# Performance work log

Hardware: AMD Instinct MI355X
Metric: run time of the kernel (lower is better)

The kernel has to match this reference:

```python
import jax, jax.numpy as jnp
import numpy as np

D = 1024      # model dim (used for theta exponent and 1/sqrt(d) scale)
D_H = 128     # head dim


def make_theta():
    # theta[i] = 10 ** (-2*(i-1)/d), each value repeated twice -> length d_H
    i = np.repeat(np.arange(D_H // 2), 2)
    return jnp.asarray(10.0 ** (-2.0 * (i - 1) / D), dtype=jnp.float32)


def rotation(x, theta):
    # x: [B, T, d_H]; positions are 1..T (source uses arange(1, T+1))
    B, T, dh = x.shape
    idx = jnp.arange(1, T + 1, dtype=x.dtype)[:, None]          # [T, 1]
    ang = idx * theta[None, :]                                   # [T, d_H]
    cos, sin = jnp.cos(ang), jnp.sin(ang)
    # pairwise swap with sign: (x0, x1) -> (x1, -x0)
    x2 = x.reshape(B, T, dh // 2, 2)
    swapped = jnp.stack([x2[..., 1], -x2[..., 0]], axis=-1).reshape(B, T, dh)
    return x * cos + swapped * sin


def setup_inputs() -> dict:
    key = jax.random.key(0)
    kx, kq, kk, kv = jax.random.split(key, 4)
    B, T = 4, 2048
    scale = 1.0 / np.sqrt(D)
    return {
        "x": jax.random.normal(kx, (B, T, D), dtype=jnp.float32),
        "Wq": jax.random.normal(kq, (D_H, D), dtype=jnp.float32) * scale,
        "Wk": jax.random.normal(kk, (D_H, D), dtype=jnp.float32) * scale,
        "Wv": jax.random.normal(kv, (D_H, D), dtype=jnp.float32) * scale,
        "theta": make_theta(),
    }


def reference(x, Wq, Wk, Wv, theta):
    B, T, d = x.shape
    Q = jnp.einsum('btd,hd->bth', x, Wq)
    K = jnp.einsum('btd,hd->bth', x, Wk)
    V = jnp.einsum('btd,hd->bth', x, Wv)
    Q = rotation(Q, theta)
    K = rotation(K, theta)
    # scale uses model dim d (not d_H), as in the source
    scores = jnp.einsum('bqh,bkh->bqk', Q, K) * (d ** -0.5)
    causal = jnp.tril(jnp.ones((T, T), dtype=bool))
    scores = jnp.where(causal, scores, -jnp.inf)
    attn = jax.nn.softmax(scores, axis=-1)
    return jnp.einsum('bqk,bkh->bqh', attn, V)
```

## Files before the change

kernel.cpp:

```cpp
#include <hip/hip_runtime.h>
#include <math.h>

#define T_SEQ 2048
#define D_MODEL 1024
#define DH 128
#define SLOTS 288
#define FRAG_B 262144

typedef __bf16 bfx8 __attribute__((ext_vector_type(8)));
typedef float f32x4 __attribute__((ext_vector_type(4)));

union U16x8 { uint4 u4; unsigned int ui[4]; unsigned short us[8]; __bf16 bf[8]; bfx8 v; };

__device__ inline uint4 cvt8u(float4 a, float4 b) {
    U16x8 u;
    u.bf[0] = (__bf16)a.x; u.bf[1] = (__bf16)a.y; u.bf[2] = (__bf16)a.z; u.bf[3] = (__bf16)a.w;
    u.bf[4] = (__bf16)b.x; u.bf[5] = (__bf16)b.y; u.bf[6] = (__bf16)b.z; u.bf[7] = (__bf16)b.w;
    return u.u4;
}

__device__ inline int slot_base32(int qt) {
    int g = qt >> 3, j = qt & 7;
    return 4 * g * (g + 1) + j * (g + 1);
}

__global__ __launch_bounds__(256) void prep_kernel(
    const float* __restrict__ x,
    const float* __restrict__ Wq, const float* __restrict__ Wk,
    const float* __restrict__ Wv,
    __bf16* __restrict__ xF, __bf16* __restrict__ WF, int nxb)
{
    const int bi = blockIdx.x;
    const int tid = threadIdx.x;

    if (bi < nxb) {
        __shared__ __align__(16) unsigned short Xs[64 * 72];
        const int m0 = (bi >> 4) * 64;
        const int k0 = (bi & 15) * 64;
        const int row = tid >> 2, cs = (tid & 3) * 16;
        const float* xp = x + (size_t)(m0 + row) * D_MODEL + k0 + cs;
        float4 a0 = *(const float4*)xp;
        float4 a1 = *(const float4*)(xp + 4);
        float4 a2 = *(const float4*)(xp + 8);
        float4 a3 = *(const float4*)(xp + 12);
        *(uint4*)&Xs[row * 72 + cs]     = cvt8u(a0, a1);
        *(uint4*)&Xs[row * 72 + cs + 8] = cvt8u(a2, a3);
        __syncthreads();
        const int L = tid & 63;
        #pragma unroll
        for (int rr = 0; rr < 2; ++rr) {
            const int fid = rr * 4 + (tid >> 6);
            const int mtl = fid >> 1, kcl = fid & 1;
            uint4 d = *(const uint4*)&Xs[(mtl * 16 + (L & 15)) * 72 + kcl * 32 + (L >> 4) * 8];
            const size_t frag = (size_t)((m0 >> 4) + mtl) * 32 + (k0 >> 5) + kcl;
            *(uint4*)&xF[frag * 512 + L * 8] = d;
        }
    } else {
        const int i = (bi - nxb) * 256 + tid;
        const int wsel = i >> 14;
        const int i2 = i & 16383;
        const int kc = i2 >> 9, j = (i2 >> 6) & 7, ln = i2 & 63;
        const int lo = ln & 15, quad = ln >> 4;
        const float* src = (wsel == 0) ? Wq : (wsel == 1) ? Wk : Wv;
        const float* p = src + (size_t)(j * 16 + lo) * D_MODEL + kc * 32 + quad * 8;
        float4 a = *(const float4*)p;
        float4 b = *(const float4*)(p + 4);
        *(uint4*)&WF[(size_t)((wsel * 32 + kc) * 8 + j) * 512 + ln * 8] = cvt8u(a, b);
    }
}

__global__ __launch_bounds__(64) void qkv_kernel(
    const __bf16* __restrict__ xF, const __bf16* __restrict__ WF,
    const float* __restrict__ theta,
    __bf16* __restrict__ QF, __bf16* __restrict__ KF, __bf16* __restrict__ VF)
{
    __shared__ __align__(16) unsigned short T[32 * 136];

    const int bx = blockIdx.x;
    const int ln = threadIdx.x;
    const int lo = ln & 15, quad = ln >> 4;

    if (bx < 2048) {
        const int wsel01 = bx >> 10;
        const int sub = (bx >> 8) & 3;
        const int iq = sub >> 1, jh = sub & 1;
        const int mt = bx & 255;
        const int mt16 = mt * 2 + iq;

        const __bf16* WFp = WF + (size_t)wsel01 * (32 * 8 * 512) + (size_t)jh * (4 * 512);
        const size_t xb = (size_t)mt16 * 32;

        bfx8 xA = *(const bfx8*)&xF[(xb + 0) * 512 + ln * 8];
        bfx8 xB = *(const bfx8*)&xF[(xb + 1) * 512 + ln * 8];
        bfx8 wA[4], wB[4];
        #pragma unroll
        for (int jl = 0; jl < 4; ++jl) {
            wA[jl] = *(const bfx8*)&WFp[(size_t)jl * 512 + ln * 8];
            wB[jl] = *(const bfx8*)&WFp[(size_t)(8 + jl) * 512 + ln * 8];
        }

        f32x4 acc[4];
        #pragma unroll
        for (int jl = 0; jl < 4; ++jl) acc[jl] = (f32x4)(0.f);

        for (int kc = 0; kc < 32; kc += 2) {
            const int kpA = (kc + 2 < 32) ? kc + 2 : kc;
            #pragma unroll
            for (int jl = 0; jl < 4; ++jl) {
                acc[jl] = __builtin_amdgcn_mfma_f32_16x16x32_bf16(xA, wA[jl], acc[jl], 0, 0, 0);
                wA[jl] = *(const bfx8*)&WFp[((size_t)kpA * 8 + jl) * 512 + ln * 8];
            }
            xA = *(const bfx8*)&xF[(xb + kpA) * 512 + ln * 8];
            const int kpB = (kc + 3 < 32) ? kc + 3 : kc + 1;
            #pragma unroll
            for (int jl = 0; jl < 4; ++jl) {
                acc[jl] = __builtin_amdgcn_mfma_f32_16x16x32_bf16(xB, wB[jl], acc[jl], 0, 0, 0);
                wB[jl] = *(const bfx8*)&WFp[((size_t)kpB * 8 + jl) * 512 + ln * 8];
            }
            xB = *(const bfx8*)&xF[(xb + kpB) * 512 + ln * 8];
        }

        const int b = mt16 >> 7;
        const int t16 = mt16 & 127;
        const int mloc16 = t16 * 16;
        __bf16* dstP = (wsel01 == 0 ? QF : KF) + (size_t)b * FRAG_B;

        #pragma unroll
        for (int jl = 0; jl < 4; ++jl) {
            const int j = jh * 4 + jl;
            const int h = j * 16 + lo;
            const float th = theta[h];
            #pragma unroll
            for (int r = 0; r < 4; ++r) {
                const int pos = mloc16 + quad * 4 + r + 1;
                float v = acc[jl][r];
                float partner = __shfl_xor(v, 1, 64);
                float ang = (float)pos * th;
                float rev = ang * 0.15915494309189535f;
                rev -= floorf(rev);
                float sn = __builtin_amdgcn_sinf(rev);
                float cs = __builtin_amdgcn_cosf(rev);
                float res = (h & 1) ? (v * cs - partner * sn)
                                    : (v * cs + partner * sn);
                U16x8 u; u.bf[0] = (__bf16)res;
                T[(quad * 4 + r) * 136 + h] = u.us[0];
            }
        }
        #pragma unroll
        for (int c4l = 0; c4l < 2; ++c4l) {
            const int c4 = jh * 2 + c4l;
            uint4 d = *(const uint4*)&T[(ln & 15) * 136 + c4 * 32 + (ln >> 4) * 8];
            *(uint4*)&dstP[(size_t)(t16 * 4 + c4) * 512 + ln * 8] = d;
        }
    } else {
        const int r2 = bx - 2048;
        const int jh = r2 >> 8;
        const int mt = r2 & 255;
        const int mt16 = mt * 2;

        const __bf16* WFp = WF + (size_t)2 * (32 * 8 * 512) + (size_t)jh * (4 * 512);
        const size_t xb0 = (size_t)mt16 * 32, xb1 = xb0 + 32;

        bfx8 xA[2], xB[2], wA[4], wB[4];
        xA[0] = *(const bfx8*)&xF[(xb0 + 0) * 512 + ln * 8];
        xA[1] = *(const bfx8*)&xF[(xb1 + 0) * 512 + ln * 8];
        xB[0] = *(const bfx8*)&xF[(xb0 + 1) * 512 + ln * 8];
        xB[1] = *(const bfx8*)&xF[(xb1 + 1) * 512 + ln * 8];
        #pragma unroll
        for (int jl = 0; jl < 4; ++jl) {
            wA[jl] = *(const bfx8*)&WFp[(size_t)jl * 512 + ln * 8];
            wB[jl] = *(const bfx8*)&WFp[(size_t)(8 + jl) * 512 + ln * 8];
        }

        f32x4 acc[2][4];
        #pragma unroll
        for (int iq = 0; iq < 2; ++iq)
            #pragma unroll
            for (int jl = 0; jl < 4; ++jl) acc[iq][jl] = (f32x4)(0.f);

        for (int kc = 0; kc < 32; kc += 2) {
            const int kpA = (kc + 2 < 32) ? kc + 2 : kc;
            #pragma unroll
            for (int jl = 0; jl < 4; ++jl) {
                acc[0][jl] = __builtin_amdgcn_mfma_f32_16x16x32_bf16(xA[0], wA[jl], acc[0][jl], 0, 0, 0);
                acc[1][jl] = __builtin_amdgcn_mfma_f32_16x16x32_bf16(xA[1], wA[jl], acc[1][jl], 0, 0, 0);
                wA[jl] = *(const bfx8*)&WFp[((size_t)kpA * 8 + jl) * 512 + ln * 8];
            }
            xA[0] = *(const bfx8*)&xF[(xb0 + kpA) * 512 + ln * 8];
            xA[1] = *(const bfx8*)&xF[(xb1 + kpA) * 512 + ln * 8];
            const int kpB = (kc + 3 < 32) ? kc + 3 : kc + 1;
            #pragma unroll
            for (int jl = 0; jl < 4; ++jl) {
                acc[0][jl] = __builtin_amdgcn_mfma_f32_16x16x32_bf16(xB[0], wB[jl], acc[0][jl], 0, 0, 0);
                acc[1][jl] = __builtin_amdgcn_mfma_f32_16x16x32_bf16(xB[1], wB[jl], acc[1][jl], 0, 0, 0);
                wB[jl] = *(const bfx8*)&WFp[((size_t)kpB * 8 + jl) * 512 + ln * 8];
            }
            xB[0] = *(const bfx8*)&xF[(xb0 + kpB) * 512 + ln * 8];
            xB[1] = *(const bfx8*)&xF[(xb1 + kpB) * 512 + ln * 8];
        }

        const int b = mt >> 6;
        const int kt32 = mt & 63;
        #pragma unroll
        for (int iq = 0; iq < 2; ++iq)
            #pragma unroll
            for (int jl = 0; jl < 4; ++jl) {
                const int j = jh * 4 + jl;
                #pragma unroll
                for (int r = 0; r < 4; ++r) {
                    U16x8 u; u.bf[0] = (__bf16)acc[iq][jl][r];
                    T[(iq * 16 + quad * 4 + r) * 136 + j * 16 + lo] = u.us[0];
                }
            }
        __bf16* dstP = VF + (size_t)b * FRAG_B;
        #pragma unroll
        for (int jl = 0; jl < 4; ++jl) {
            const int j = jh * 4 + jl;
            U16x8 u;
            #pragma unroll
            for (int e = 0; e < 8; ++e)
                u.us[e] = T[((ln >> 4) * 8 + e) * 136 + j * 16 + (ln & 15)];
            *(uint4*)&dstP[(size_t)(kt32 * 8 + j) * 512 + ln * 8] = u.u4;
        }
    }
}

__global__ __launch_bounds__(128) void attn_partial_kernel(
    const __bf16* __restrict__ QF, const __bf16* __restrict__ KF,
    const __bf16* __restrict__ VF,
    __bf16* __restrict__ Opb, float* __restrict__ Ll)
{
    const int bxx = blockIdx.x;
    const int b = bxx >> 1;
    const int qt = (int)blockIdx.y * 2 + (bxx & 1);
    const int c = blockIdx.z;
    const int qbase = qt * 32;
    const int kstart = c << 8;
    if (kstart > qbase) return;
    const int nt = min(8, (qbase + 32 - kstart) >> 5);

    __shared__ __align__(16) unsigned short Pw[2][1280];
    __shared__ float RedO[2 * 8 * 4 * 64];
    __shared__ float RedL[2 * 4 * 64];

    const int tid = threadIdx.x;
    const int w = tid >> 6;
    const int ln = tid & 63;
    const int lo = ln & 15, quad = ln >> 4;
    const int hi8 = quad * 8;

    const __bf16* QFb = QF + (size_t)b * FRAG_B;
    const __bf16* KFb = KF + (size_t)b * FRAG_B;
    const __bf16* VFb = VF + (size_t)b * FRAG_B;

    bfx8 qf[2][4];
    #pragma unroll
    for (int iq = 0; iq < 2; ++iq)
        #pragma unroll
        for (int c4 = 0; c4 < 4; ++c4)
            qf[iq][c4] = *(const bfx8*)&QFb[(size_t)((qt * 2 + iq) * 4 + c4) * 512 + ln * 8];

    f32x4 O[2][8];
    #pragma unroll
    for (int iq = 0; iq < 2; ++iq)
        #pragma unroll
        for (int j = 0; j < 8; ++j) O[iq][j] = (f32x4)(0.f);
    float lsum[2][4];
    #pragma unroll
    for (int iq = 0; iq < 2; ++iq)
        #pragma unroll
        for (int r = 0; r < 4; ++r) lsum[iq][r] = 0.f;

    bfx8 kcur[2][4], knxt[2][4];
    {
        const int kf0 = (kstart + w * 32) >> 4;
        #pragma unroll
        for (int jj = 0; jj < 2; ++jj)
            #pragma unroll
            for (int c4 = 0; c4 < 4; ++c4)
                kcur[jj][c4] = *(const bfx8*)&KFb[(size_t)((kf0 + jj) * 4 + c4) * 512 + ln * 8];
    }

    for (int kt = w; kt < nt; kt += 2) {
        const int k0 = kstart + kt * 32;
        bfx8 vf[8];
        #pragma unroll
        for (int j = 0; j < 8; ++j)
            vf[j] = *(const bfx8*)&VFb[(size_t)((k0 >> 5) * 8 + j) * 512 + ln * 8];
        if (kt + 2 < nt) {
            const int kn16 = (k0 + 64) >> 4;
            #pragma unroll
            for (int jj = 0; jj < 2; ++jj)
                #pragma unroll
                for (int c4 = 0; c4 < 4; ++c4)
                    knxt[jj][c4] = *(const bfx8*)&KFb[(size_t)((kn16 + jj) * 4 + c4) * 512 + ln * 8];
        }

        f32x4 s4[2][2];
        #pragma unroll
        for (int iq = 0; iq < 2; ++iq)
            #pragma unroll
            for (int jj = 0; jj < 2; ++jj) s4[iq][jj] = (f32x4)(0.f);
        #pragma unroll
        for (int c4 = 0; c4 < 4; ++c4)
            #pragma unroll
            for (int iq = 0; iq < 2; ++iq)
                #pragma unroll
                for (int jj = 0; jj < 2; ++jj)
                    s4[iq][jj] = __builtin_amdgcn_mfma_f32_16x16x32_bf16(qf[iq][c4], kcur[jj][c4], s4[iq][jj], 0, 0, 0);

        const bool needMask = (k0 + 31 > qbase);
        #pragma unroll
        for (int iq = 0; iq < 2; ++iq)
            #pragma unroll
            for (int jj = 0; jj < 2; ++jj)
                #pragma unroll
                for (int r = 0; r < 4; ++r) {
                    const int col = k0 + jj * 16 + lo;
                    const int row = qbase + iq * 16 + quad * 4 + r;
                    float p = __expf(s4[iq][jj][r] * 0.03125f);
                    if (needMask && col > row) p = 0.f;
                    lsum[iq][r] += p;
                    U16x8 u; u.bf[0] = (__bf16)p;
                    Pw[w][iq * 640 + (quad * 4 + r) * 40 + jj * 16 + lo] = u.us[0];
                }

        bfx8 pf0 = *(const bfx8*)&Pw[w][lo * 40 + hi8];
        bfx8 pf1 = *(const bfx8*)&Pw[w][640 + lo * 40 + hi8];
        #pragma unroll
        for (int j = 0; j < 8; ++j) {
            O[0][j] = __builtin_amdgcn_mfma_f32_16x16x32_bf16(pf0, vf[j], O[0][j], 0, 0, 0);
            O[1][j] = __builtin_amdgcn_mfma_f32_16x16x32_bf16(pf1, vf[j], O[1][j], 0, 0, 0);
        }

        #pragma unroll
        for (int jj = 0; jj < 2; ++jj)
            #pragma unroll
            for (int c4 = 0; c4 < 4; ++c4) kcur[jj][c4] = knxt[jj][c4];
    }

    #pragma unroll
    for (int off = 1; off < 16; off <<= 1)
        #pragma unroll
        for (int iq = 0; iq < 2; ++iq)
            #pragma unroll
            for (int r = 0; r < 4; ++r) lsum[iq][r] += __shfl_xor(lsum[iq][r], off, 64);

    if (w == 1) {
        #pragma unroll
        for (int iq = 0; iq < 2; ++iq)
            #pragma unroll
            for (int j = 0; j < 8; ++j)
                #pragma unroll
                for (int r = 0; r < 4; ++r)
                    RedO[((iq * 8 + j) * 4 + r) * 64 + ln] = O[iq][j][r];
        #pragma unroll
        for (int iq = 0; iq < 2; ++iq)
            #pragma unroll
            for (int r = 0; r < 4; ++r)
                RedL[(iq * 4 + r) * 64 + ln] = lsum[iq][r];
    }
    __syncthreads();
    if (w == 0) {
        #pragma unroll
        for (int iq = 0; iq < 2; ++iq)
            #pragma unroll
            for (int j = 0; j < 8; ++j)
                #pragma unroll
                for (int r = 0; r < 4; ++r)
                    O[iq][j][r] += RedO[((iq * 8 + j) * 4 + r) * 64 + ln];
        #pragma unroll
        for (int iq = 0; iq < 2; ++iq)
            #pragma unroll
            for (int r = 0; r < 4; ++r)
                lsum[iq][r] += RedL[(iq * 4 + r) * 64 + ln];

        const size_t sb = (size_t)b * SLOTS + slot_base32(qt) + c;
        #pragma unroll
        for (int iq = 0; iq < 2; ++iq)
            #pragma unroll
            for (int j = 0; j < 8; ++j) {
                U16x8 u;
                u.bf[0] = (__bf16)O[iq][j][0]; u.bf[1] = (__bf16)O[iq][j][1];
                u.bf[2] = (__bf16)O[iq][j][2]; u.bf[3] = (__bf16)O[iq][j][3];
                *(uint2*)&Opb[((sb * 2 + iq) * 8 + j) * 256 + ln * 4] = make_uint2(u.ui[0], u.ui[1]);
            }
        if (lo == 0) {
            #pragma unroll
            for (int iq = 0; iq < 2; ++iq)
                #pragma unroll
                for (int r = 0; r < 4; ++r)
                    Ll[sb * 32 + iq * 16 + quad * 4 + r] = lsum[iq][r];
        }
    }
}

__global__ __launch_bounds__(128) void attn_merge_kernel(
    const __bf16* __restrict__ Opb, const float* __restrict__ Ll,
    float* __restrict__ out)
{
    const int qt = blockIdx.x, b = blockIdx.y, jh2 = blockIdx.z;
    const int g = qt >> 3, nc = g + 1;
    const size_t base = (size_t)b * SLOTS + slot_base32(qt);

    __shared__ float Lsh[8][32];
    const int tid = threadIdx.x;
    const int iq = tid >> 6, ln = tid & 63;
    const int lo = ln & 15, quad = ln >> 4;

    for (int idx = tid; idx < nc * 32; idx += 128)
        Lsh[idx >> 5][idx & 31] = Ll[(base + (idx >> 5)) * 32 + (idx & 31)];
    __syncthreads();

    float acc[4][4];
    #pragma unroll
    for (int jl = 0; jl < 4; ++jl)
        #pragma unroll
        for (int r = 0; r < 4; ++r) acc[jl][r] = 0.f;

    for (int cc = 0; cc < nc; ++cc) {
        #pragma unroll
        for (int jl = 0; jl < 4; ++jl) {
            const int j = jh2 * 4 + jl;
            uint2 d = *(const uint2*)&Opb[(((base + cc) * 2 + iq) * 8 + j) * 256 + ln * 4];
            U16x8 u; u.ui[0] = d.x; u.ui[1] = d.y;
            #pragma unroll
            for (int r = 0; r < 4; ++r) acc[jl][r] += (float)u.bf[r];
        }
    }

    #pragma unroll
    for (int r = 0; r < 4; ++r) {
        const int row = iq * 16 + quad * 4 + r;
        float l = 0.f;
        for (int cc = 0; cc < nc; ++cc) l += Lsh[cc][row];
        const float rl = 1.0f / l;
        #pragma unroll
        for (int jl = 0; jl < 4; ++jl) {
            const int j = jh2 * 4 + jl;
            out[((size_t)b * T_SEQ + qt * 32 + row) * DH + j * 16 + lo] = acc[jl][r] * rl;
        }
    }
}

extern "C" void kernel_launch(void* const* d_in, const int* in_sizes, int n_in,
                              void* d_out, int out_size, void* d_ws, size_t ws_size,
                              hipStream_t stream) {
    const float* x     = (const float*)d_in[0];
    const float* Wq    = (const float*)d_in[1];
    const float* Wk    = (const float*)d_in[2];
    const float* Wv    = (const float*)d_in[3];
    const float* theta = (const float*)d_in[4];
    float* out = (float*)d_out;

    const int M = in_sizes[0] / D_MODEL;
    const int B = M / T_SEQ;

    __bf16* xF  = (__bf16*)d_ws;
    __bf16* WF  = xF + (size_t)M * D_MODEL;
    __bf16* QF  = WF + (size_t)3 * 32 * 8 * 512;
    __bf16* KF  = QF + (size_t)B * FRAG_B;
    __bf16* VF  = KF + (size_t)B * FRAG_B;
    __bf16* Opb = VF + (size_t)B * FRAG_B;
    float*  Ll  = (float*)(Opb + (size_t)B * SLOTS * 2 * 8 * 256);

    const int nxb = (M / 64) * 16;
    prep_kernel<<<dim3(nxb + 192), 256, 0, stream>>>(x, Wq, Wk, Wv, xF, WF, nxb);
    qkv_kernel<<<dim3(2048 + 512), 64, 0, stream>>>(xF, WF, theta, QF, KF, VF);
    attn_partial_kernel<<<dim3(2 * B, T_SEQ / 64, 8), 128, 0, stream>>>(QF, KF, VF, Opb, Ll);
    attn_merge_kernel<<<dim3(T_SEQ / 32, B, 2), 128, 0, stream>>>(Opb, Ll, out);
}
```

Baseline: 122.1 us.

## Fuse four-stage pipeline into one persistent cooperative kernel with grid syncs

Replaces the four separate launches (prep, QKV projection, partial attention, merge) with a single cooperative persistent kernel. Each phase is split into tasks that blocks or waves take in a strided loop, and phases are separated by grid.sync. This removes per-launch overhead and the idle gaps between kernels. In exchange, the whole grid waits at each barrier, the work is spread across a fixed 256 or 512 blocks, and register pressure rises under launch_bounds(256,2). The old four-kernel path remains as a fallback if the cooperative launch fails.

```diff
diff --git a/kernel.cpp b/kernel.cpp
--- a/kernel.cpp
+++ b/kernel.cpp
@@ -1,5 +1,8 @@
 #include <hip/hip_runtime.h>
+#include <hip/hip_cooperative_groups.h>
 #include <math.h>
+
+namespace cg = cooperative_groups;
 
 #define T_SEQ 2048
 #define D_MODEL 1024
@@ -23,6 +26,7 @@
     int g = qt >> 3, j = qt & 7;
     return 4 * g * (g + 1) + j * (g + 1);
 }
+
 
 __global__ __launch_bounds__(256) void prep_kernel(
     const float* __restrict__ x,
@@ -443,6 +447,413 @@
     }
 }
 
+
+__device__ __forceinline__ void qkv_task(
+    int t, unsigned short* T,
+    const __bf16* __restrict__ xF, const __bf16* __restrict__ WF,
+    const float* __restrict__ theta,
+    __bf16* __restrict__ QF, __bf16* __restrict__ KF, __bf16* __restrict__ VF,
+    int ln, int lo, int quad)
+{
+    if (t < 2048) {
+        const int wsel01 = t >> 10;
+        const int sub = (t >> 8) & 3;
+        const int iq = sub >> 1, jh = sub & 1;
+        const int mt = t & 255;
+        const int mt16 = mt * 2 + iq;
+
+        const __bf16* WFp = WF + (size_t)wsel01 * (32 * 8 * 512) + (size_t)jh * (4 * 512);
+        const size_t xb = (size_t)mt16 * 32;
+
+        bfx8 xA = *(const bfx8*)&xF[(xb + 0) * 512 + ln * 8];
+        bfx8 xB = *(const bfx8*)&xF[(xb + 1) * 512 + ln * 8];
+        bfx8 wA[4], wB[4];
+        #pragma unroll
+        for (int jl = 0; jl < 4; ++jl) {
+            wA[jl] = *(const bfx8*)&WFp[(size_t)jl * 512 + ln * 8];
+            wB[jl] = *(const bfx8*)&WFp[(size_t)(8 + jl) * 512 + ln * 8];
+        }
+
+        f32x4 acc[4];
+        #pragma unroll
+        for (int jl = 0; jl < 4; ++jl) acc[jl] = (f32x4)(0.f);
+
+        for (int kc = 0; kc < 32; kc += 2) {
+            const int kpA = (kc + 2 < 32) ? kc + 2 : kc;
+            #pragma unroll
+            for (int jl = 0; jl < 4; ++jl) {
+                acc[jl] = __builtin_amdgcn_mfma_f32_16x16x32_bf16(xA, wA[jl], acc[jl], 0, 0, 0);
+                wA[jl] = *(const bfx8*)&WFp[((size_t)kpA * 8 + jl) * 512 + ln * 8];
+            }
+            xA = *(const bfx8*)&xF[(xb + kpA) * 512 + ln * 8];
+            const int kpB = (kc + 3 < 32) ? kc + 3 : kc + 1;
+            #pragma unroll
+            for (int jl = 0; jl < 4; ++jl) {
+                acc[jl] = __builtin_amdgcn_mfma_f32_16x16x32_bf16(xB, wB[jl], acc[jl], 0, 0, 0);
+                wB[jl] = *(const bfx8*)&WFp[((size_t)kpB * 8 + jl) * 512 + ln * 8];
+            }
+            xB = *(const bfx8*)&xF[(xb + kpB) * 512 + ln * 8];
+        }
+
+        const int b = mt16 >> 7;
+        const int t16 = mt16 & 127;
+        const int mloc16 = t16 * 16;
+        __bf16* dstP = (wsel01 == 0 ? QF : KF) + (size_t)b * FRAG_B;
+
+        #pragma unroll
+        for (int jl = 0; jl < 4; ++jl) {
+            const int j = jh * 4 + jl;
+            const int h = j * 16 + lo;
+            const float th = theta[h];
+            #pragma unroll
+            for (int r = 0; r < 4; ++r) {
+                const int pos = mloc16 + quad * 4 + r + 1;
+                float v = acc[jl][r];
+                float partner = __shfl_xor(v, 1, 64);
+                float ang = (float)pos * th;
+                float rev = ang * 0.15915494309189535f;
+                rev -= floorf(rev);
+                float sn = __builtin_amdgcn_sinf(rev);
+                float cs = __builtin_amdgcn_cosf(rev);
+                float res = (h & 1) ? (v * cs - partner * sn)
+                                    : (v * cs + partner * sn);
+                U16x8 u; u.bf[0] = (__bf16)res;
+                T[(quad * 4 + r) * 136 + h] = u.us[0];
+            }
+        }
+        #pragma unroll
+        for (int c4l = 0; c4l < 2; ++c4l) {
+            const int c4 = jh * 2 + c4l;
+            uint4 d = *(const uint4*)&T[(ln & 15) * 136 + c4 * 32 + (ln >> 4) * 8];
+            *(uint4*)&dstP[(size_t)(t16 * 4 + c4) * 512 + ln * 8] = d;
+        }
+    } else {
+        const int r2 = t - 2048;
+        const int jh = r2 >> 8;
+        const int mt = r2 & 255;
+        const int mt16 = mt * 2;
+
+        const __bf16* WFp = WF + (size_t)2 * (32 * 8 * 512) + (size_t)jh * (4 * 512);
+        const size_t xb0 = (size_t)mt16 * 32, xb1 = xb0 + 32;
+
+        bfx8 xA[2], xB[2], wA[4], wB[4];
+        xA[0] = *(const bfx8*)&xF[(xb0 + 0) * 512 + ln * 8];
+        xA[1] = *(const bfx8*)&xF[(xb1 + 0) * 512 + ln * 8];
+        xB[0] = *(const bfx8*)&xF[(xb0 + 1) * 512 + ln * 8];
+        xB[1] = *(const bfx8*)&xF[(xb1 + 1) * 512 + ln * 8];
+        #pragma unroll
+        for (int jl = 0; jl < 4; ++jl) {
+            wA[jl] = *(const bfx8*)&WFp[(size_t)jl * 512 + ln * 8];
+            wB[jl] = *(const bfx8*)&WFp[(size_t)(8 + jl) * 512 + ln * 8];
+        }
+
+        f32x4 acc[2][4];
+        #pragma unroll
+        for (int iq = 0; iq < 2; ++iq)
+            #pragma unroll
+            for (int jl = 0; jl < 4; ++jl) acc[iq][jl] = (f32x4)(0.f);
+
+        for (int kc = 0; kc < 32; kc += 2) {
+            const int kpA = (kc + 2 < 32) ? kc + 2 : kc;
+            #pragma unroll
+            for (int jl = 0; jl < 4; ++jl) {
+                acc[0][jl] = __builtin_amdgcn_mfma_f32_16x16x32_bf16(xA[0], wA[jl], acc[0][jl], 0, 0, 0);
+                acc[1][jl] = __builtin_amdgcn_mfma_f32_16x16x32_bf16(xA[1], wA[jl], acc[1][jl], 0, 0, 0);
+                wA[jl] = *(const bfx8*)&WFp[((size_t)kpA * 8 + jl) * 512 + ln * 8];
+            }
+            xA[0] = *(const bfx8*)&xF[(xb0 + kpA) * 512 + ln * 8];
+            xA[1] = *(const bfx8*)&xF[(xb1 + kpA) * 512 + ln * 8];
+            const int kpB = (kc + 3 < 32) ? kc + 3 : kc + 1;
+            #pragma unroll
+            for (int jl = 0; jl < 4; ++jl) {
+                acc[0][jl] = __builtin_amdgcn_mfma_f32_16x16x32_bf16(xB[0], wB[jl], acc[0][jl], 0, 0, 0);
+                acc[1][jl] = __builtin_amdgcn_mfma_f32_16x16x32_bf16(xB[1], wB[jl], acc[1][jl], 0, 0, 0);
+                wB[jl] = *(const bfx8*)&WFp[((size_t)kpB * 8 + jl) * 512 + ln * 8];
+            }
+            xB[0] = *(const bfx8*)&xF[(xb0 + kpB) * 512 + ln * 8];
+            xB[1] = *(const bfx8*)&xF[(xb1 + kpB) * 512 + ln * 8];
+        }
+
+        const int b = mt >> 6;
+        const int kt32 = mt & 63;
+        #pragma unroll
+        for (int iq = 0; iq < 2; ++iq)
+            #pragma unroll
+            for (int jl = 0; jl < 4; ++jl) {
+                const int j = jh * 4 + jl;
+                #pragma unroll
+                for (int r = 0; r < 4; ++r) {
+                    U16x8 u; u.bf[0] = (__bf16)acc[iq][jl][r];
+                    T[(iq * 16 + quad * 4 + r) * 136 + j * 16 + lo] = u.us[0];
+                }
+            }
+        __bf16* dstP = VF + (size_t)b * FRAG_B;
+        #pragma unroll
+        for (int jl = 0; jl < 4; ++jl) {
+            const int j = jh * 4 + jl;
+            U16x8 u;
+            #pragma unroll
+            for (int e = 0; e < 8; ++e)
+                u.us[e] = T[((ln >> 4) * 8 + e) * 136 + j * 16 + (ln & 15)];
+            *(uint4*)&dstP[(size_t)(kt32 * 8 + j) * 512 + ln * 8] = u.u4;
+        }
+    }
+}
+
+__global__ __launch_bounds__(256, 2) void fused_kernel(
+    const float* __restrict__ x,
+    const float* __restrict__ Wq, const float* __restrict__ Wk,
+    const float* __restrict__ Wv, const float* __restrict__ theta,
+    __bf16* __restrict__ xF, __bf16* __restrict__ WF,
+    __bf16* __restrict__ QF, __bf16* __restrict__ KF, __bf16* __restrict__ VF,
+    __bf16* __restrict__ Opb, float* __restrict__ Ll,
+    float* __restrict__ out)
+{
+    __shared__ __align__(16) unsigned char SMEM[34816];
+    cg::grid_group grid = cg::this_grid();
+
+    const int nblk = gridDim.x;
+    const int bid = blockIdx.x;
+    const int tid = threadIdx.x;
+    const int w = tid >> 6;
+    const int ln = tid & 63;
+    const int lo = ln & 15, quad = ln >> 4;
+    const int wid = bid * 4 + w;
+
+    {
+        unsigned short* Xs = (unsigned short*)SMEM;
+        for (int task = bid; task < 2048 + 192; task += nblk) {
+            if (task < 2048) {
+                const int m0 = (task >> 4) * 64;
+                const int k0 = (task & 15) * 64;
+                const int row = tid >> 2, cs = (tid & 3) * 16;
+                const float* xp = x + (size_t)(m0 + row) * D_MODEL + k0 + cs;
+                float4 a0 = *(const float4*)xp;
+                float4 a1 = *(const float4*)(xp + 4);
+                float4 a2 = *(const float4*)(xp + 8);
+                float4 a3 = *(const float4*)(xp + 12);
+                *(uint4*)&Xs[row * 72 + cs]     = cvt8u(a0, a1);
+                *(uint4*)&Xs[row * 72 + cs + 8] = cvt8u(a2, a3);
+                __syncthreads();
+                const int L = tid & 63;
+                #pragma unroll
+                for (int rr = 0; rr < 2; ++rr) {
+                    const int fid = rr * 4 + (tid >> 6);
+                    const int mtl = fid >> 1, kcl = fid & 1;
+                    uint4 d = *(const uint4*)&Xs[(mtl * 16 + (L & 15)) * 72 + kcl * 32 + (L >> 4) * 8];
+                    const size_t frag = (size_t)((m0 >> 4) + mtl) * 32 + (k0 >> 5) + kcl;
+                    *(uint4*)&xF[frag * 512 + L * 8] = d;
+                }
+                __syncthreads();
+            } else {
+                const int i = (task - 2048) * 256 + tid;
+                const int wsel = i >> 14;
+                const int i2 = i & 16383;
+                const int kc = i2 >> 9, j = (i2 >> 6) & 7, l2 = i2 & 63;
+                const int lo2 = l2 & 15, q2 = l2 >> 4;
+                const float* src = (wsel == 0) ? Wq : (wsel == 1) ? Wk : Wv;
+                const float* p = src + (size_t)(j * 16 + lo2) * D_MODEL + kc * 32 + q2 * 8;
+                float4 a = *(const float4*)p;
+                float4 b = *(const float4*)(p + 4);
+                *(uint4*)&WF[(size_t)((wsel * 32 + kc) * 8 + j) * 512 + l2 * 8] = cvt8u(a, b);
+            }
+        }
+    }
+    __threadfence();
+    grid.sync();
+    __threadfence();
+
+    {
+        unsigned short* T = (unsigned short*)SMEM + (size_t)w * (32 * 136);
+        const int nw = nblk * 4;
+        for (int t = wid; t < 2560; t += nw)
+            qkv_task(t, T, xF, WF, theta, QF, KF, VF, ln, lo, quad);
+    }
+    __threadfence();
+    grid.sync();
+    __threadfence();
+
+    {
+        const int cls = bid & 7;
+        const int b = cls >> 1, parity = cls & 1;
+        const int strideR = (nblk >> 3) * 4;
+        unsigned short* Pw = (unsigned short*)SMEM + (size_t)w * 1280;
+        const int hi8 = quad * 8;
+
+        const __bf16* QFb = QF + (size_t)b * FRAG_B;
+        const __bf16* KFb = KF + (size_t)b * FRAG_B;
+        const __bf16* VFb = VF + (size_t)b * FRAG_B;
+
+        for (int rk = (bid >> 3) * 4 + w; rk < 144; rk += strideR) {
+            int qt2 = 0, accb = 0;
+            while (true) { int ncg = (qt2 >> 2) + 1; if (rk < accb + ncg) break; accb += ncg; ++qt2; }
+            const int c = rk - accb;
+            const int qt = qt2 * 2 + parity;
+            const int qbase = qt * 32;
+            const int kstart = c << 8;
+            const int nt = min(8, (qbase + 32 - kstart) >> 5);
+
+            bfx8 qf[2][4];
+            #pragma unroll
+            for (int iq = 0; iq < 2; ++iq)
+                #pragma unroll
+                for (int c4 = 0; c4 < 4; ++c4)
+                    qf[iq][c4] = *(const bfx8*)&QFb[(size_t)((qt * 2 + iq) * 4 + c4) * 512 + ln * 8];
+
+            f32x4 O[2][8];
+            #pragma unroll
+            for (int iq = 0; iq < 2; ++iq)
+                #pragma unroll
+                for (int j = 0; j < 8; ++j) O[iq][j] = (f32x4)(0.f);
+            float lsum[2][4];
+            #pragma unroll
+            for (int iq = 0; iq < 2; ++iq)
+                #pragma unroll
+                for (int r = 0; r < 4; ++r) lsum[iq][r] = 0.f;
+
+            bfx8 kcur[2][4], knxt[2][4];
+            #pragma unroll
+            for (int jj = 0; jj < 2; ++jj)
+                #pragma unroll
+                for (int c4 = 0; c4 < 4; ++c4)
+                    kcur[jj][c4] = *(const bfx8*)&KFb[(size_t)(((kstart >> 4) + jj) * 4 + c4) * 512 + ln * 8];
+
+            for (int kt = 0; kt < nt; ++kt) {
+                const int k0 = kstart + kt * 32;
+                bfx8 vf[8];
+                #pragma unroll
+                for (int j = 0; j < 8; ++j)
+                    vf[j] = *(const bfx8*)&VFb[(size_t)((k0 >> 5) * 8 + j) * 512 + ln * 8];
+                if (kt + 1 < nt) {
+                    const int kn16 = (k0 + 32) >> 4;
+                    #pragma unroll
+                    for (int jj = 0; jj < 2; ++jj)
+                        #pragma unroll
+                        for (int c4 = 0; c4 < 4; ++c4)
+                            knxt[jj][c4] = *(const bfx8*)&KFb[(size_t)((kn16 + jj) * 4 + c4) * 512 + ln * 8];
+                }
+
+                f32x4 s4[2][2];
+                #pragma unroll
+                for (int iq = 0; iq < 2; ++iq)
+                    #pragma unroll
+                    for (int jj = 0; jj < 2; ++jj) s4[iq][jj] = (f32x4)(0.f);
+                #pragma unroll
+                for (int c4 = 0; c4 < 4; ++c4)
+                    #pragma unroll
+                    for (int iq = 0; iq < 2; ++iq)
+                        #pragma unroll
+                        for (int jj = 0; jj < 2; ++jj)
+                            s4[iq][jj] = __builtin_amdgcn_mfma_f32_16x16x32_bf16(qf[iq][c4], kcur[jj][c4], s4[iq][jj], 0, 0, 0);
+
+                const bool needMask = (k0 + 31 > qbase);
+                #pragma unroll
+                for (int iq = 0; iq < 2; ++iq)
+                    #pragma unroll
+                    for (int jj = 0; jj < 2; ++jj)
+                        #pragma unroll
+                        for (int r = 0; r < 4; ++r) {
+                            const int col = k0 + jj * 16 + lo;
+                            const int row = qbase + iq * 16 + quad * 4 + r;
+                            float p = __expf(s4[iq][jj][r] * 0.03125f);
+                            if (needMask && col > row) p = 0.f;
+                            lsum[iq][r] += p;
+                            U16x8 u; u.bf[0] = (__bf16)p;
+                            Pw[iq * 640 + (quad * 4 + r) * 40 + jj * 16 + lo] = u.us[0];
+                        }
+
+                bfx8 pf0 = *(const bfx8*)&Pw[lo * 40 + hi8];
+                bfx8 pf1 = *(const bfx8*)&Pw[640 + lo * 40 + hi8];
+                #pragma unroll
+                for (int j = 0; j < 8; ++j) {
+                    O[0][j] = __builtin_amdgcn_mfma_f32_16x16x32_bf16(pf0, vf[j], O[0][j], 0, 0, 0);
+                    O[1][j] = __builtin_amdgcn_mfma_f32_16x16x32_bf16(pf1, vf[j], O[1][j], 0, 0, 0);
+                }
+
+                #pragma unroll
+                for (int jj = 0; jj < 2; ++jj)
+                    #pragma unroll
+                    for (int c4 = 0; c4 < 4; ++c4) kcur[jj][c4] = knxt[jj][c4];
+            }
+
+            #pragma unroll
+            for (int off = 1; off < 16; off <<= 1)
+                #pragma unroll
+                for (int iq = 0; iq < 2; ++iq)
+                    #pragma unroll
+                    for (int r = 0; r < 4; ++r) lsum[iq][r] += __shfl_xor(lsum[iq][r], off, 64);
+
+            const size_t sb = (size_t)b * SLOTS + slot_base32(qt) + c;
+            #pragma unroll
+            for (int iq = 0; iq < 2; ++iq)
+                #pragma unroll
+                for (int j = 0; j < 8; ++j) {
+                    U16x8 u;
+                    u.bf[0] = (__bf16)O[iq][j][0]; u.bf[1] = (__bf16)O[iq][j][1];
+                    u.bf[2] = (__bf16)O[iq][j][2]; u.bf[3] = (__bf16)O[iq][j][3];
+                    *(uint2*)&Opb[((sb * 2 + iq) * 8 + j) * 256 + ln * 4] = make_uint2(u.ui[0], u.ui[1]);
+                }
+            if (lo == 0) {
+                #pragma unroll
+                for (int iq = 0; iq < 2; ++iq)
+                    #pragma unroll
+                    for (int r = 0; r < 4; ++r)
+                        Ll[sb * 32 + iq * 16 + quad * 4 + r] = lsum[iq][r];
+            }
+        }
+    }
+    __threadfence();
+    grid.sync();
+    __threadfence();
+
+    for (int mb = bid; mb < 256; mb += nblk) {
+        const int qt = mb >> 2, b = mb & 3;
+        const int nc = (qt >> 3) + 1;
+        const size_t base = (size_t)b * SLOTS + slot_base32(qt);
+
+        float* Lsh = (float*)SMEM;
+        for (int idx = tid; idx < nc * 32; idx += 256)
+            Lsh[idx] = Ll[(base + (idx >> 5)) * 32 + (idx & 31)];
+        __syncthreads();
+
+        const int jh2 = tid >> 7;
+        const int iq = (tid >> 6) & 1;
+        const int l2 = tid & 63;
+        const int lo2 = l2 & 15, q2 = l2 >> 4;
+
+        float acc[4][4];
+        #pragma unroll
+        for (int jl = 0; jl < 4; ++jl)
+            #pragma unroll
+            for (int r = 0; r < 4; ++r) acc[jl][r] = 0.f;
+
+        for (int cc = 0; cc < nc; ++cc) {
+            #pragma unroll
+            for (int jl = 0; jl < 4; ++jl) {
+                const int j = jh2 * 4 + jl;
+                uint2 d = *(const uint2*)&Opb[(((base + cc) * 2 + iq) * 8 + j) * 256 + l2 * 4];
+                U16x8 u; u.ui[0] = d.x; u.ui[1] = d.y;
+                #pragma unroll
+                for (int r = 0; r < 4; ++r) acc[jl][r] += (float)u.bf[r];
+            }
+        }
+
+        #pragma unroll
+        for (int r = 0; r < 4; ++r) {
+            const int row = iq * 16 + q2 * 4 + r;
+            float l = 0.f;
+            for (int cc = 0; cc < nc; ++cc) l += Lsh[cc * 32 + row];
+            const float rl = 1.0f / l;
+            #pragma unroll
+            for (int jl = 0; jl < 4; ++jl) {
+                const int j = jh2 * 4 + jl;
+                out[((size_t)b * T_SEQ + qt * 32 + row) * DH + j * 16 + lo2] = acc[jl][r] * rl;
+            }
+        }
+        __syncthreads();
+    }
+}
+
 extern "C" void kernel_launch(void* const* d_in, const int* in_sizes, int n_in,
                               void* d_out, int out_size, void* d_ws, size_t ws_size,
                               hipStream_t stream) {
@@ -464,9 +875,31 @@
     __bf16* Opb = VF + (size_t)B * FRAG_B;
     float*  Ll  = (float*)(Opb + (size_t)B * SLOTS * 2 * 8 * 256);
 
-    const int nxb = (M / 64) * 16;
-    prep_kernel<<<dim3(nxb + 192), 256, 0, stream>>>(x, Wq, Wk, Wv, xF, WF, nxb);
-    qkv_kernel<<<dim3(2048 + 512), 64, 0, stream>>>(xF, WF, theta, QF, KF, VF);
-    attn_partial_kernel<<<dim3(2 * B, T_SEQ / 64, 8), 128, 0, stream>>>(QF, KF, VF, Opb, Ll);
-    attn_merge_kernel<<<dim3(T_SEQ / 32, B, 2), 128, 0, stream>>>(Opb, Ll, out);
+    static int coopGrid = -1;
+    if (coopGrid < 0) {
+        int attr = 0, mb = 0;
+        hipError_t e1 = hipDeviceGetAttribute(&attr, hipDeviceAttributeCooperativeLaunch, 0);
+        hipError_t e2 = hipOccupancyMaxActiveBlocksPerMultiprocessor(&mb, fused_kernel, 256, 0);
+        coopGrid = (e1 == hipSuccess && attr != 0 && e2 == hipSuccess && mb >= 1)
+                   ? ((mb >= 2) ? 512 : 256) : 0;
+    }
+
+    bool launched = false;
+    if (coopGrid > 0) {
+        void* args[] = { (void*)&x, (void*)&Wq, (void*)&Wk, (void*)&Wv, (void*)&theta,
+                         (void*)&xF, (void*)&WF, (void*)&QF, (void*)&KF, (void*)&VF,
+                         (void*)&Opb, (void*)&Ll, (void*)&out };
+        hipError_t err = hipLaunchCooperativeKernel((void*)fused_kernel, dim3(coopGrid),
+                                                    dim3(256), args, 0, stream);
+        launched = (err == hipSuccess);
+        if (!launched) coopGrid = 0;
+    }
+
+    if (!launched) {
+        const int nxb = (M / 64) * 16;
+        prep_kernel<<<dim3(nxb + 192), 256, 0, stream>>>(x, Wq, Wk, Wv, xF, WF, nxb);
+        qkv_kernel<<<dim3(2048 + 512), 64, 0, stream>>>(xF, WF, theta, QF, KF, VF);
+        attn_partial_kernel<<<dim3(2 * B, T_SEQ / 64, 8), 128, 0, stream>>>(QF, KF, VF, Opb, Ll);
+        attn_merge_kernel<<<dim3(T_SEQ / 32, B, 2), 128, 0, stream>>>(Opb, Ll, out);
+    }
 }
```

Result: slower. 364.4 us (+198.5%).

## Fuse split-K attention merge into partial kernel via last-block atomic counter

Applied to the files above, without the earlier changes.

Removes the separate merge kernel. Each partial-attention block increments a per-(batch, query-tile) atomic counter, and the last block to finish reduces all partial outputs and row sums and writes the final result. Counters are zeroed inside the prep kernel. This removes a kernel launch and its tail gap, but the merge now runs serialized inside one block per tile and adds atomics and fences.

```diff
diff --git a/kernel.cpp b/kernel.cpp
--- a/kernel.cpp
+++ b/kernel.cpp
@@ -28,7 +28,8 @@
     const float* __restrict__ x,
     const float* __restrict__ Wq, const float* __restrict__ Wk,
     const float* __restrict__ Wv,
-    __bf16* __restrict__ xF, __bf16* __restrict__ WF, int nxb)
+    __bf16* __restrict__ xF, __bf16* __restrict__ WF,
+    unsigned int* __restrict__ Cnt, int nxb)
 {
     const int bi = blockIdx.x;
     const int tid = threadIdx.x;
@@ -56,6 +57,7 @@
             *(uint4*)&xF[frag * 512 + L * 8] = d;
         }
     } else {
+        if (bi == nxb) Cnt[tid] = 0;
         const int i = (bi - nxb) * 256 + tid;
         const int wsel = i >> 14;
         const int i2 = i & 16383;
@@ -228,7 +230,8 @@
 __global__ __launch_bounds__(128) void attn_partial_kernel(
     const __bf16* __restrict__ QF, const __bf16* __restrict__ KF,
     const __bf16* __restrict__ VF,
-    __bf16* __restrict__ Opb, float* __restrict__ Ll)
+    __bf16* __restrict__ Opb, float* __restrict__ Ll,
+    unsigned int* __restrict__ Cnt, float* __restrict__ out)
 {
     const int bxx = blockIdx.x;
     const int b = bxx >> 1;
@@ -238,10 +241,12 @@
     const int kstart = c << 8;
     if (kstart > qbase) return;
     const int nt = min(8, (qbase + 32 - kstart) >> 5);
+    const int ncq = (qt >> 3) + 1;
 
     __shared__ __align__(16) unsigned short Pw[2][1280];
     __shared__ float RedO[2 * 8 * 4 * 64];
     __shared__ float RedL[2 * 4 * 64];
+    __shared__ int isLastSh;
 
     const int tid = threadIdx.x;
     const int w = tid >> 6;
@@ -393,52 +398,59 @@
                     Ll[sb * 32 + iq * 16 + quad * 4 + r] = lsum[iq][r];
         }
     }
-}
-
-__global__ __launch_bounds__(128) void attn_merge_kernel(
-    const __bf16* __restrict__ Opb, const float* __restrict__ Ll,
-    float* __restrict__ out)
-{
-    const int qt = blockIdx.x, b = blockIdx.y, jh2 = blockIdx.z;
-    const int g = qt >> 3, nc = g + 1;
-    const size_t base = (size_t)b * SLOTS + slot_base32(qt);
-
-    __shared__ float Lsh[8][32];
-    const int tid = threadIdx.x;
-    const int iq = tid >> 6, ln = tid & 63;
-    const int lo = ln & 15, quad = ln >> 4;
-
-    for (int idx = tid; idx < nc * 32; idx += 128)
-        Lsh[idx >> 5][idx & 31] = Ll[(base + (idx >> 5)) * 32 + (idx & 31)];
+
     __syncthreads();
-
-    float acc[4][4];
-    #pragma unroll
-    for (int jl = 0; jl < 4; ++jl)
-        #pragma unroll
-        for (int r = 0; r < 4; ++r) acc[jl][r] = 0.f;
-
-    for (int cc = 0; cc < nc; ++cc) {
-        #pragma unroll
-        for (int jl = 0; jl < 4; ++jl) {
-            const int j = jh2 * 4 + jl;
-            uint2 d = *(const uint2*)&Opb[(((base + cc) * 2 + iq) * 8 + j) * 256 + ln * 4];
-            U16x8 u; u.ui[0] = d.x; u.ui[1] = d.y;
-            #pragma unroll
-            for (int r = 0; r < 4; ++r) acc[jl][r] += (float)u.bf[r];
-        }
-    }
-
-    #pragma unroll
-    for (int r = 0; r < 4; ++r) {
-        const int row = iq * 16 + quad * 4 + r;
-        float l = 0.f;
-        for (int cc = 0; cc < nc; ++cc) l += Lsh[cc][row];
-        const float rl = 1.0f / l;
-        #pragma unroll
-        for (int jl = 0; jl < 4; ++jl) {
-            const int j = jh2 * 4 + jl;
-            out[((size_t)b * T_SEQ + qt * 32 + row) * DH + j * 16 + lo] = acc[jl][r] * rl;
+    if (tid == 0) {
+        __threadfence();
+        unsigned int old = atomicAdd(&Cnt[b * 64 + qt], 1u);
+        isLastSh = (old == (unsigned int)(ncq - 1)) ? 1 : 0;
+    }
+    __syncthreads();
+    if (!isLastSh) return;
+    __threadfence();
+
+    {
+        const size_t base = (size_t)b * SLOTS + slot_base32(qt);
+        float* Lsh = RedO;
+        for (int idx = tid; idx < ncq * 32; idx += 128)
+            Lsh[idx] = Ll[(base + (idx >> 5)) * 32 + (idx & 31)];
+        __syncthreads();
+
+        const int iqm = tid >> 6;
+        const int l2 = tid & 63;
+        const int lo2 = l2 & 15, q2 = l2 >> 4;
+
+        #pragma unroll
+        for (int jh2 = 0; jh2 < 2; ++jh2) {
+            float accm[4][4];
+            #pragma unroll
+            for (int jl = 0; jl < 4; ++jl)
+                #pragma unroll
+                for (int r = 0; r < 4; ++r) accm[jl][r] = 0.f;
+
+            for (int cc = 0; cc < ncq; ++cc) {
+                #pragma unroll
+                for (int jl = 0; jl < 4; ++jl) {
+                    const int j = jh2 * 4 + jl;
+                    uint2 d = *(const uint2*)&Opb[(((base + cc) * 2 + iqm) * 8 + j) * 256 + l2 * 4];
+                    U16x8 u; u.ui[0] = d.x; u.ui[1] = d.y;
+                    #pragma unroll
+                    for (int r = 0; r < 4; ++r) accm[jl][r] += (float)u.bf[r];
+                }
+            }
+
+            #pragma unroll
+            for (int r = 0; r < 4; ++r) {
+                const int row = iqm * 16 + q2 * 4 + r;
+                float l = 0.f;
+                for (int cc = 0; cc < ncq; ++cc) l += Lsh[cc * 32 + row];
+                const float rl = 1.0f / l;
+                #pragma unroll
+                for (int jl = 0; jl < 4; ++jl) {
+                    const int j = jh2 * 4 + jl;
+                    out[((size_t)b * T_SEQ + qt * 32 + row) * DH + j * 16 + lo2] = accm[jl][r] * rl;
+                }
+            }
         }
     }
 }
@@ -463,10 +475,10 @@
     __bf16* VF  = KF + (size_t)B * FRAG_B;
     __bf16* Opb = VF + (size_t)B * FRAG_B;
     float*  Ll  = (float*)(Opb + (size_t)B * SLOTS * 2 * 8 * 256);
+    unsigned int* Cnt = (unsigned int*)(Ll + (size_t)B * SLOTS * 32);
 
     const int nxb = (M / 64) * 16;
-    prep_kernel<<<dim3(nxb + 192), 256, 0, stream>>>(x, Wq, Wk, Wv, xF, WF, nxb);
+    prep_kernel<<<dim3(nxb + 192), 256, 0, stream>>>(x, Wq, Wk, Wv, xF, WF, Cnt, nxb);
     qkv_kernel<<<dim3(2048 + 512), 64, 0, stream>>>(xF, WF, theta, QF, KF, VF);
-    attn_partial_kernel<<<dim3(2 * B, T_SEQ / 64, 8), 128, 0, stream>>>(QF, KF, VF, Opb, Ll);
-    attn_merge_kernel<<<dim3(T_SEQ / 32, B, 2), 128, 0, stream>>>(Opb, Ll, out);
-}
+    attn_partial_kernel<<<dim3(2 * B, T_SEQ / 64, 8), 128, 0, stream>>>(QF, KF, VF, Opb, Ll, Cnt, out);
+}
```

Result: slower. 170.9 us (+40.0%).
